# Optimization experiments

Hardware: AMD Instinct MI355X
Metric: run time of the kernel (lower is better)

## Reference

```python
import jax, jax.numpy as jnp
import numpy as np

IOU_THRESHOLD = 0.5


def setup_inputs() -> dict:
    key = jax.random.key(0)
    k1, k2, k3 = jax.random.split(key, 3)
    B, N = 4, 8192
    # valid boxes: top-left in [0,200), width/height in [1,51)
    xy = jax.random.uniform(k1, (B, N, 2), dtype=jnp.float32) * 200.0
    wh = jax.random.uniform(k2, (B, N, 2), dtype=jnp.float32) * 50.0 + 1.0
    boxes = jnp.concatenate([xy, xy + wh], axis=-1)  # [B,N,4] (x1,y1,x2,y2)
    scores = jax.random.uniform(k3, (B, N), dtype=jnp.float32)
    return {"boxes": boxes, "scores": scores}


def _soft_nms_single(boxes, scores):
    # boxes: [N,4], scores: [N]
    x1, y1, x2, y2 = boxes[:, 0], boxes[:, 1], boxes[:, 2], boxes[:, 3]
    inter_w = jnp.maximum(0.0, jnp.minimum(x2[:, None], x2[None, :]) - jnp.maximum(x1[:, None], x1[None, :]))
    inter_h = jnp.maximum(0.0, jnp.minimum(y2[:, None], y2[None, :]) - jnp.maximum(y1[:, None], y1[None, :]))
    inter = inter_w * inter_h  # [N,N]
    area = (x2 - x1) * (y2 - y1)  # [N]
    union = area[:, None] + area[None, :] - inter
    iou = inter / union  # [N,N]
    weight = jnp.exp(-iou / IOU_THRESHOLD)  # [N,N]
    adjusted = weight @ scores  # [N] : adjusted_scores[i] = sum_j w[i,j]*s[j]
    w = jax.nn.softmax(adjusted, axis=0)  # [N]
    return w @ boxes  # [4]


def reference(boxes, scores):
    return jax.vmap(_soft_nms_single)(boxes, scores)  # [B,4]
```

## Files before the change

kernel.cpp:

```cpp
#include <hip/hip_runtime.h>
#include <hip/hip_bf16.h>

#define BATCH   4
#define NBOX    8192
#define BLOCK   256
#define TSZ     256
#define NT      (NBOX / TSZ)
#define NPAIRS  (NT * (NT + 1) / 2)
#define NBINS   2048
#define SUBS    8
#define SUBSZ   (NBOX / SUBS)
#define STH     512

__device__ __forceinline__ float bf2f(unsigned short u) {
    union { unsigned int i; float f; } c;
    c.i = ((unsigned int)u) << 16;
    return c.f;
}

__device__ __forceinline__ bool box_plausible(float x1, float y1, float x2, float y2) {
    bool ok = (x1 == x1) && (y1 == y1) && (x2 == x2) && (y2 == y2);
    ok = ok && fabsf(x1) < 1e4f && fabsf(y1) < 1e4f && fabsf(x2) < 1e4f && fabsf(y2) < 1e4f;
    ok = ok && x1 >= -1.0f && x1 <= 300.0f && y1 >= -1.0f && y1 <= 300.0f;
    const float w = x2 - x1, h = y2 - y1;
    ok = ok && w >= -0.1f && w <= 80.0f && h >= -0.1f && h <= 80.0f;
    return ok;
}

__device__ __forceinline__ bool wave_probe_is_f32(const void* boxes_raw) {
    const int lane = threadIdx.x & 63;
    const float* bf = (const float*)boxes_raw;
    const bool okf = box_plausible(bf[lane * 4 + 0], bf[lane * 4 + 1],
                                   bf[lane * 4 + 2], bf[lane * 4 + 3]);
    const unsigned short* bh = (const unsigned short*)boxes_raw;
    const bool okh = box_plausible(bf2f(bh[lane * 4 + 0]), bf2f(bh[lane * 4 + 1]),
                                   bf2f(bh[lane * 4 + 2]), bf2f(bh[lane * 4 + 3]));
    const unsigned long long mf = __ballot(okf);
    const unsigned long long mh = __ballot(okh);
    return __popcll(mf) >= __popcll(mh);
}

__device__ __forceinline__ float4 load_box(const void* boxes_raw, size_t idx, bool isf32) {
    if (isf32) {
        return reinterpret_cast<const float4*>(boxes_raw)[idx];
    } else {
        const ushort4 u = reinterpret_cast<const ushort4*>(boxes_raw)[idx];
        return make_float4(bf2f(u.x), bf2f(u.y), bf2f(u.z), bf2f(u.w));
    }
}

__device__ __forceinline__ float load_score(const void* scores_raw, size_t idx, bool isf32) {
    return isf32 ? ((const float*)scores_raw)[idx]
                 : bf2f(((const unsigned short*)scores_raw)[idx]);
}

__device__ __forceinline__ int x1_bin(float x1) {
    const int bb = (int)(x1 * 8.0f);
    return min(NBINS - 1, max(0, bb));
}

#define CEXP (-2.8853900817779268f)

__device__ __forceinline__ float pair_weight(
    float ix1, float iy1, float ix2, float iy2, float iarea,
    const float4& bj, float jarea)
{
    float w = fminf(ix2, bj.z) - fmaxf(ix1, bj.x);
    float h = fminf(iy2, bj.w) - fmaxf(iy1, bj.y);
    w = fmaxf(w, 0.0f);
    h = fmaxf(h, 0.0f);
    const float inter = w * h;
    const float uni   = iarea + jarea - inter;
    const float arg   = (CEXP * inter) * __builtin_amdgcn_rcpf(uni);
    return __builtin_amdgcn_exp2f(arg);
}

__global__ __launch_bounds__(STH) void sort_kernel(
    const void* __restrict__ boxes_raw, const void* __restrict__ scores_raw,
    float4* __restrict__ sboxes, float* __restrict__ sscores,
    float* __restrict__ adj,
    float* __restrict__ minx1c, float* __restrict__ maxx2c,
    int* __restrict__ pairlist, int* __restrict__ count)
{
    __shared__ int hist[NBINS];
    __shared__ int bmax[NBINS];
    __shared__ int hist2[NBINS];
    __shared__ int wsum[STH / 64];
    __shared__ float sminT[NT], smaxT[NT];
    __shared__ int scnt;

    const int b    = blockIdx.x / SUBS;
    const int sub  = blockIdx.x % SUBS;
    const int tid  = threadIdx.x;
    const int lane = tid & 63;
    const int wv   = tid >> 6;
    const bool isf32 = wave_probe_is_f32(boxes_raw);
    const size_t base = (size_t)b * NBOX;

#pragma unroll
    for (int i = 0; i < NBINS / STH; i++) {
        hist[i * STH + tid]  = 0;
        bmax[i * STH + tid]  = 0;
        hist2[i * STH + tid] = 0;
    }
    if (tid == 0) scnt = 0;
    {
        const size_t z = (size_t)blockIdx.x * 1024;
        adj[z + tid] = 0.0f;
        adj[z + STH + tid] = 0.0f;
    }
    __syncthreads();

#pragma unroll
    for (int k = 0; k < NBOX / STH; k++) {
        const float4 bx = load_box(boxes_raw, base + k * STH + tid, isf32);
        const int bin = x1_bin(bx.x);
        atomicAdd(&hist[bin], 1);
        atomicMax(&bmax[bin], __float_as_int(bx.z));
    }
    for (int i = tid; i < sub * SUBSZ; i += STH) {
        const float4 bx = load_box(boxes_raw, base + i, isf32);
        atomicAdd(&hist2[x1_bin(bx.x)], 1);
    }
    __syncthreads();

    {
        int tot[4], cum[4];
        int run = 0;
#pragma unroll
        for (int i = 0; i < 4; i++) {
            tot[i] = hist[tid * 4 + i];
            run += tot[i]; cum[i] = run;
        }
        int v = run;
#pragma unroll
        for (int d = 1; d < 64; d <<= 1) {
            const int u = __shfl_up(v, d);
            if (lane >= d) v += u;
        }
        if (lane == 63) wsum[wv] = v;
        __syncthreads();
        int wb = 0;
        for (int w = 0; w < wv; w++) wb += wsum[w];
        const int tb = wb + v - run;
#pragma unroll
        for (int i = 0; i < 4; i++) {
            const int bin = tid * 4 + i;
            const int e = tb + cum[i] - tot[i];
            const int m = hist2[bin];
            hist[bin]  = e;
            hist2[bin] = e + m;
        }
    }
    __syncthreads();

    if (tid < NT) {
        int p = tid * TSZ;
        int lo = 0, hi = NBINS - 1;
        while (lo < hi) { const int mid = (lo + hi + 1) >> 1;
                          if (hist[mid] <= p) lo = mid; else hi = mid - 1; }
        const int Bf = lo;
        p = tid * TSZ + TSZ - 1;
        lo = 0; hi = NBINS - 1;
        while (lo < hi) { const int mid = (lo + hi + 1) >> 1;
                          if (hist[mid] <= p) lo = mid; else hi = mid - 1; }
        const int Bl = lo;
        int mb = 0;
        for (int q = Bf; q <= Bl; q++) mb = max(mb, bmax[q]);
        const float mn = (float)Bf * 0.125f;
        const float mx = __int_as_float(mb);
        sminT[tid] = mn; smaxT[tid] = mx;
        if (sub == 0) {
            minx1c[b * NT + tid] = mn;
            maxx2c[b * NT + tid] = mx;
        }
    }
    __syncthreads();

    if (sub == 0) {
        for (int q = tid; q < NPAIRS; q += STH) {
            int p = q, it = 0;
            while (p >= NT - it) { p -= NT - it; it++; }
            const int jt = it + p;
            const bool live = !((smaxT[it] < sminT[jt]) || (smaxT[jt] < sminT[it]));
            if (live) {
                const int idx = atomicAdd(&scnt, 1);
                pairlist[b * NPAIRS + idx] = (it << 8) | jt;
            }
        }
    }

#pragma unroll
    for (int k = 0; k < SUBSZ / STH; k++) {
        const int i = sub * SUBSZ + k * STH + tid;
        const float4 bx = load_box(boxes_raw, base + i, isf32);
        const float  sc = load_score(scores_raw, base + i, isf32);
        const int pos = atomicAdd(&hist2[x1_bin(bx.x)], 1);
        sboxes[base + pos]  = bx;
        sscores[base + pos] = sc;
    }

    __syncthreads();
    if (sub == 0 && tid == 0) count[b] = scnt;
}

__global__ __launch_bounds__(BLOCK, 4) void soft_nms_adj_kernel(
    const float4* __restrict__ sboxes,
    const float* __restrict__ sscores,
    const int* __restrict__ pairlist,
    const int* __restrict__ count,
    float* __restrict__ adj)
{
    __shared__ float4 sbox[TSZ];
    __shared__ float2 sas[TSZ];
    __shared__ float  srow[4][TSZ];

    const int bid = blockIdx.x;
    const int b   = bid / NPAIRS;
    const int p   = bid % NPAIRS;
    if (p >= count[b]) return;
    const int pr = pairlist[b * NPAIRS + p];
    const int it = pr >> 8, jt = pr & 255;

    const int tid  = threadIdx.x;
    const int lane = tid & 63;
    const int wv   = tid >> 6;
    const size_t base = (size_t)b * NBOX;

    {
        const int jg = jt * TSZ + tid;
        const float4 uj = sboxes[base + jg];
        sbox[tid] = uj;
        sas[tid]  = make_float2((uj.z - uj.x) * (uj.w - uj.y), sscores[base + jg]);
    }

    float rx1[4], ry1[4], rx2[4], ry2[4], rar[4], rsc[4], accr[4];
#pragma unroll
    for (int k = 0; k < 4; k++) {
        const int ig = it * TSZ + k * 64 + lane;
        const float4 ui = sboxes[base + ig];
        rx1[k] = ui.x; ry1[k] = ui.y; rx2[k] = ui.z; ry2[k] = ui.w;
        rar[k] = (ui.z - ui.x) * (ui.w - ui.y);
        rsc[k] = sscores[base + ig];
        accr[k] = 0.0f;
    }

    __syncthreads();

    const int wvbase = wv * 64;

    if (it == jt) {
#pragma unroll 2
        for (int t = 0; t < 64; t++) {
            const int idx = wvbase + ((lane + t) & 63);
            const float4 bj = sbox[idx];
            const float2 as = sas[idx];
#pragma unroll
            for (int k = 0; k < 4; k++) {
                const float e = pair_weight(rx1[k], ry1[k], rx2[k], ry2[k], rar[k], bj, as.x);
                accr[k] = fmaf(e, as.y, accr[k]);
            }
        }
    } else {
        float accc = 0.0f;
#pragma unroll 2
        for (int t = 0; t < 64; t++) {
            const int idx = wvbase + ((lane + t) & 63);
            const float4 bj = sbox[idx];
            const float2 as = sas[idx];
            const float e0 = pair_weight(rx1[0], ry1[0], rx2[0], ry2[0], rar[0], bj, as.x);
            const float e1 = pair_weight(rx1[1], ry1[1], rx2[1], ry2[1], rar[1], bj, as.x);
            const float e2 = pair_weight(rx1[2], ry1[2], rx2[2], ry2[2], rar[2], bj, as.x);
            const float e3 = pair_weight(rx1[3], ry1[3], rx2[3], ry2[3], rar[3], bj, as.x);
            accr[0] = fmaf(e0, as.y, accr[0]);
            accr[1] = fmaf(e1, as.y, accr[1]);
            accr[2] = fmaf(e2, as.y, accr[2]);
            accr[3] = fmaf(e3, as.y, accr[3]);
            const float c = fmaf(e0, rsc[0], fmaf(e1, rsc[1], fmaf(e2, rsc[2], e3 * rsc[3])));
            accc += __shfl(c, (lane - t) & 63);
        }
        atomicAdd(&adj[base + jt * TSZ + wvbase + lane], accc);
    }

#pragma unroll
    for (int k = 0; k < 4; k++) srow[wv][k * 64 + lane] = accr[k];
    __syncthreads();
    {
        const float rs = srow[0][tid] + srow[1][tid] + srow[2][tid] + srow[3][tid];
        atomicAdd(&adj[base + it * TSZ + tid], rs);
    }
}

#define FBLK 1024
__global__ __launch_bounds__(FBLK) void soft_nms_finish_kernel(
    const float4* __restrict__ sboxes,
    const float* __restrict__ sscores,
    const float* __restrict__ adj,
    const float* __restrict__ minx1c, const float* __restrict__ maxx2c,
    const void* __restrict__ boxes_raw,
    void* __restrict__ out)
{
    constexpr int K  = NBOX / FBLK;
    constexpr int NW = FBLK / 64;
    __shared__ float sminx[NT], smaxx[NT], ssumT[NT], scorr[NT];
    __shared__ float smax_[NW];
    __shared__ float sred[NW][5];

    const int b    = blockIdx.x;
    const int tid  = threadIdx.x;
    const int lane = tid & 63;
    const int wv   = tid >> 6;
    const size_t base = (size_t)b * NBOX;

    const bool isf32 = wave_probe_is_f32(boxes_raw);

    if (tid < NT) {
        sminx[tid] = minx1c[b * NT + tid];
        smaxx[tid] = maxx2c[b * NT + tid];
    }
#pragma unroll
    for (int tt = 0; tt < 2; tt++) {
        const int T = wv * 2 + tt;
        float sm = 0.0f;
#pragma unroll
        for (int q = 0; q < 4; q++) sm += sscores[base + T * TSZ + q * 64 + lane];
#pragma unroll
        for (int off = 32; off > 0; off >>= 1) sm += __shfl_down(sm, off);
        if (lane == 0) ssumT[T] = sm;
    }
    __syncthreads();
    if (tid < NT) {
        float c = 0.0f;
        for (int T2 = 0; T2 < NT; T2++) {
            const bool skip = (smaxx[tid] < sminx[T2]) || (smaxx[T2] < sminx[tid]);
            if (skip) c += ssumT[T2];
        }
        scorr[tid] = c;
    }
    __syncthreads();

    float av[K];
    float m = -3.4e38f;
#pragma unroll
    for (int k = 0; k < K; k++) {
        const int r = k * FBLK + tid;
        av[k] = adj[base + r] + scorr[r >> 8];
        m = fmaxf(m, av[k]);
    }
#pragma unroll
    for (int off = 32; off > 0; off >>= 1)
        m = fmaxf(m, __shfl_down(m, off));
    if (lane == 0) smax_[wv] = m;
    __syncthreads();
    float M = smax_[0];
#pragma unroll
    for (int w = 1; w < NW; w++) M = fmaxf(M, smax_[w]);

    const float L2E = 1.4426950408889634f;
    float es = 0.0f, s0 = 0.0f, s1 = 0.0f, s2 = 0.0f, s3 = 0.0f;
#pragma unroll
    for (int k = 0; k < K; k++) {
        const float e = __builtin_amdgcn_exp2f((av[k] - M) * L2E);
        const float4 u = sboxes[base + k * FBLK + tid];
        es += e;
        s0 += e * u.x;
        s1 += e * u.y;
        s2 += e * u.z;
        s3 += e * u.w;
    }
#pragma unroll
    for (int off = 32; off > 0; off >>= 1) {
        es += __shfl_down(es, off);
        s0 += __shfl_down(s0, off);
        s1 += __shfl_down(s1, off);
        s2 += __shfl_down(s2, off);
        s3 += __shfl_down(s3, off);
    }
    if (lane == 0) {
        sred[wv][0] = es; sred[wv][1] = s0; sred[wv][2] = s1;
        sred[wv][3] = s2; sred[wv][4] = s3;
    }
    __syncthreads();
    if (tid == 0) {
        float ES = 0.0f, o[4] = {0.0f, 0.0f, 0.0f, 0.0f};
#pragma unroll
        for (int w = 0; w < NW; w++) {
            ES   += sred[w][0];
            o[0] += sred[w][1];
            o[1] += sred[w][2];
            o[2] += sred[w][3];
            o[3] += sred[w][4];
        }
        const float inv = 1.0f / ES;
        if (isf32) {
            float* of = (float*)out;
            for (int c = 0; c < 4; c++) of[b * 4 + c] = o[c] * inv;
        } else {
            __hip_bfloat16* oh = (__hip_bfloat16*)out;
            for (int c = 0; c < 4; c++) oh[b * 4 + c] = __float2bfloat16(o[c] * inv);
        }
    }
}

extern "C" void kernel_launch(void* const* d_in, const int* in_sizes, int n_in,
                              void* d_out, int out_size, void* d_ws, size_t ws_size,
                              hipStream_t stream) {
    const void* boxes_raw  = d_in[0];
    const void* scores_raw = d_in[1];

    char* w = (char*)d_ws;
    float4* sboxes   = (float4*)w;                 w += (size_t)BATCH * NBOX * 16;
    float*  sscores  = (float*)w;                  w += (size_t)BATCH * NBOX * 4;
    float*  adj      = (float*)w;                  w += (size_t)BATCH * NBOX * 4;
    float*  minx1c   = (float*)w;                  w += (size_t)BATCH * NT * 4;
    float*  maxx2c   = (float*)w;                  w += (size_t)BATCH * NT * 4;
    int*    pairlist = (int*)w;                    w += (size_t)BATCH * NPAIRS * 4;
    int*    count    = (int*)w;

    sort_kernel<<<dim3(BATCH * SUBS), dim3(STH), 0, stream>>>(
        boxes_raw, scores_raw, sboxes, sscores, adj, minx1c, maxx2c, pairlist, count);
    soft_nms_adj_kernel<<<dim3(BATCH * NPAIRS), dim3(BLOCK), 0, stream>>>(
        sboxes, sscores, pairlist, count, adj);
    soft_nms_finish_kernel<<<dim3(BATCH), dim3(FBLK), 0, stream>>>(
        sboxes, sscores, adj, minx1c, maxx2c, boxes_raw, d_out);
}
```

Measured before the change: 121.9 us.

## Sort boxes by x2 and skip non-overlapping row groups in off-diagonal tiles

Switches the bucket sort key from x1 to x2, so tile bounds become a min-x1 per tile and a bin-derived max-x2. In off-diagonal tiles the kernel finds leading 64-row groups whose max x2 lies below the column tile's min x1. Those pairs have zero IoU and weight 1, so their contribution is added in closed form as score sums instead of evaluated pairwise. A templated loop then runs only over the remaining row groups, cutting exp and divide work at the cost of extra shuffles and code variants.

```diff
diff --git a/kernel.cpp b/kernel.cpp
--- a/kernel.cpp
+++ b/kernel.cpp
@@ -1,5 +1,6 @@
 #include <hip/hip_runtime.h>
 #include <hip/hip_bf16.h>
+#include <type_traits>
 
 #define BATCH   4
 #define NBOX    8192
@@ -54,8 +55,8 @@
                  : bf2f(((const unsigned short*)scores_raw)[idx]);
 }
 
-__device__ __forceinline__ int x1_bin(float x1) {
-    const int bb = (int)(x1 * 8.0f);
+__device__ __forceinline__ int key_bin(float v) {
+    const int bb = (int)(v * 8.0f);
     return min(NBINS - 1, max(0, bb));
 }
 
@@ -83,7 +84,7 @@
     int* __restrict__ pairlist, int* __restrict__ count)
 {
     __shared__ int hist[NBINS];
-    __shared__ int bmax[NBINS];
+    __shared__ int bmin[NBINS];
     __shared__ int hist2[NBINS];
     __shared__ int wsum[STH / 64];
     __shared__ float sminT[NT], smaxT[NT];
@@ -100,7 +101,7 @@
 #pragma unroll
     for (int i = 0; i < NBINS / STH; i++) {
         hist[i * STH + tid]  = 0;
-        bmax[i * STH + tid]  = 0;
+        bmin[i * STH + tid]  = 0x7f800000;
         hist2[i * STH + tid] = 0;
     }
     if (tid == 0) scnt = 0;
@@ -111,16 +112,15 @@
     }
     __syncthreads();
 
+    const int sublim = sub * SUBSZ;
 #pragma unroll
     for (int k = 0; k < NBOX / STH; k++) {
-        const float4 bx = load_box(boxes_raw, base + k * STH + tid, isf32);
-        const int bin = x1_bin(bx.x);
+        const int i = k * STH + tid;
+        const float4 bx = load_box(boxes_raw, base + i, isf32);
+        const int bin = key_bin(bx.z);
         atomicAdd(&hist[bin], 1);
-        atomicMax(&bmax[bin], __float_as_int(bx.z));
-    }
-    for (int i = tid; i < sub * SUBSZ; i += STH) {
-        const float4 bx = load_box(boxes_raw, base + i, isf32);
-        atomicAdd(&hist2[x1_bin(bx.x)], 1);
+        atomicMin(&bmin[bin], __float_as_int(bx.x));
+        if (i < sublim) atomicAdd(&hist2[bin], 1);
     }
     __syncthreads();
 
@@ -165,10 +165,9 @@
         while (lo < hi) { const int mid = (lo + hi + 1) >> 1;
                           if (hist[mid] <= p) lo = mid; else hi = mid - 1; }
         const int Bl = lo;
-        int mb = 0;
-        for (int q = Bf; q <= Bl; q++) mb = max(mb, bmax[q]);
-        const float mn = (float)Bf * 0.125f;
-        const float mx = __int_as_float(mb);
+        float mn = 3.4e38f;
+        for (int q = Bf; q <= Bl; q++) mn = fminf(mn, __int_as_float(bmin[q]));
+        const float mx = (float)(Bl + 1) * 0.125f;
         sminT[tid] = mn; smaxT[tid] = mx;
         if (sub == 0) {
             minx1c[b * NT + tid] = mn;
@@ -195,7 +194,7 @@
         const int i = sub * SUBSZ + k * STH + tid;
         const float4 bx = load_box(boxes_raw, base + i, isf32);
         const float  sc = load_score(scores_raw, base + i, isf32);
-        const int pos = atomicAdd(&hist2[x1_bin(bx.x)], 1);
+        const int pos = atomicAdd(&hist2[key_bin(bx.z)], 1);
         sboxes[base + pos]  = bx;
         sscores[base + pos] = sc;
     }
@@ -209,11 +208,13 @@
     const float* __restrict__ sscores,
     const int* __restrict__ pairlist,
     const int* __restrict__ count,
+    const float* __restrict__ minx1c,
     float* __restrict__ adj)
 {
     __shared__ float4 sbox[TSZ];
     __shared__ float2 sas[TSZ];
     __shared__ float  srow[4][TSZ];
+    __shared__ float  swsum[4];
 
     const int bid = blockIdx.x;
     const int b   = bid / NPAIRS;
@@ -231,10 +232,15 @@
         const int jg = jt * TSZ + tid;
         const float4 uj = sboxes[base + jg];
         sbox[tid] = uj;
-        sas[tid]  = make_float2((uj.z - uj.x) * (uj.w - uj.y), sscores[base + jg]);
-    }
-
-    float rx1[4], ry1[4], rx2[4], ry2[4], rar[4], rsc[4], accr[4];
+        const float jsc = sscores[base + jg];
+        sas[tid]  = make_float2((uj.z - uj.x) * (uj.w - uj.y), jsc);
+        float ws = jsc;
+#pragma unroll
+        for (int off = 32; off > 0; off >>= 1) ws += __shfl_xor(ws, off);
+        if (lane == 0) swsum[wv] = ws;
+    }
+
+    float rx1[4], ry1[4], rx2[4], ry2[4], rar[4], rsc[4];
 #pragma unroll
     for (int k = 0; k < 4; k++) {
         const int ig = it * TSZ + k * 64 + lane;
@@ -242,10 +248,36 @@
         rx1[k] = ui.x; ry1[k] = ui.y; rx2[k] = ui.z; ry2[k] = ui.w;
         rar[k] = (ui.z - ui.x) * (ui.w - ui.y);
         rsc[k] = sscores[base + ig];
-        accr[k] = 0.0f;
-    }
-
-    __syncthreads();
+    }
+
+    int kstart = 0;
+    if (it != jt) {
+        const float sminJ = minx1c[b * NT + jt];
+#pragma unroll
+        for (int k = 0; k < 4; k++) {
+            const float gmax = __shfl(rx2[k], 63) + 0.125f;
+            if (kstart == k && gmax < sminJ) kstart = k + 1;
+        }
+    }
+    float ccorr = 0.0f;
+    if (kstart > 0) {
+#pragma unroll
+        for (int k = 0; k < 4; k++) {
+            if (k < kstart) {
+                float gs = rsc[k];
+#pragma unroll
+                for (int off = 32; off > 0; off >>= 1) gs += __shfl_xor(gs, off);
+                ccorr += gs;
+            }
+        }
+    }
+
+    __syncthreads();
+
+    const float tilejsum = swsum[0] + swsum[1] + swsum[2] + swsum[3];
+    float accr[4];
+#pragma unroll
+    for (int k = 0; k < 4; k++) accr[k] = (k < kstart && wv == 0) ? tilejsum : 0.0f;
 
     const int wvbase = wv * 64;
 
@@ -262,24 +294,31 @@
             }
         }
     } else {
-        float accc = 0.0f;
+        auto offd = [&](auto KSC) {
+            constexpr int KS = decltype(KSC)::value;
+            float accc = ccorr;
 #pragma unroll 2
-        for (int t = 0; t < 64; t++) {
-            const int idx = wvbase + ((lane + t) & 63);
-            const float4 bj = sbox[idx];
-            const float2 as = sas[idx];
-            const float e0 = pair_weight(rx1[0], ry1[0], rx2[0], ry2[0], rar[0], bj, as.x);
-            const float e1 = pair_weight(rx1[1], ry1[1], rx2[1], ry2[1], rar[1], bj, as.x);
-            const float e2 = pair_weight(rx1[2], ry1[2], rx2[2], ry2[2], rar[2], bj, as.x);
-            const float e3 = pair_weight(rx1[3], ry1[3], rx2[3], ry2[3], rar[3], bj, as.x);
-            accr[0] = fmaf(e0, as.y, accr[0]);
-            accr[1] = fmaf(e1, as.y, accr[1]);
-            accr[2] = fmaf(e2, as.y, accr[2]);
-            accr[3] = fmaf(e3, as.y, accr[3]);
-            const float c = fmaf(e0, rsc[0], fmaf(e1, rsc[1], fmaf(e2, rsc[2], e3 * rsc[3])));
-            accc += __shfl(c, (lane - t) & 63);
-        }
-        atomicAdd(&adj[base + jt * TSZ + wvbase + lane], accc);
+            for (int t = 0; t < 64; t++) {
+                const int idx = wvbase + ((lane + t) & 63);
+                const float4 bj = sbox[idx];
+                const float2 as = sas[idx];
+                float c = 0.0f;
+#pragma unroll
+                for (int k = KS; k < 4; ++k) {
+                    const float e = pair_weight(rx1[k], ry1[k], rx2[k], ry2[k], rar[k], bj, as.x);
+                    accr[k] = fmaf(e, as.y, accr[k]);
+                    c = fmaf(e, rsc[k], c);
+                }
+                accc += __shfl(c, (lane - t) & 63);
+            }
+            atomicAdd(&adj[base + jt * TSZ + wvbase + lane], accc);
+        };
+        switch (kstart) {
+            case 0:  offd(std::integral_constant<int, 0>{}); break;
+            case 1:  offd(std::integral_constant<int, 1>{}); break;
+            case 2:  offd(std::integral_constant<int, 2>{}); break;
+            default: offd(std::integral_constant<int, 3>{}); break;
+        }
     }
 
 #pragma unroll
@@ -420,7 +459,7 @@
     sort_kernel<<<dim3(BATCH * SUBS), dim3(STH), 0, stream>>>(
         boxes_raw, scores_raw, sboxes, sscores, adj, minx1c, maxx2c, pairlist, count);
     soft_nms_adj_kernel<<<dim3(BATCH * NPAIRS), dim3(BLOCK), 0, stream>>>(
-        sboxes, sscores, pairlist, count, adj);
+        sboxes, sscores, pairlist, count, minx1c, adj);
     soft_nms_finish_kernel<<<dim3(BATCH), dim3(FBLK), 0, stream>>>(
         sboxes, sscores, adj, minx1c, maxx2c, boxes_raw, d_out);
 }
```

Result: slower. 135.5 us (+11.1%).

## Sort boxes by x2 key and split adjacency tiles into single-wave blocks

Applied to the files above, without the earlier changes.

The sort now bins boxes by x2 instead of x1, and tile bounds come from per-bin minimum x1 and the bin's upper x2 edge. The second-prefix histogram pass is folded into the main load loop. The adjacency kernel launches one 64-thread wave per quarter of a tile pair instead of a 256-thread block. This removes __syncthreads and the shared-memory row reduction, and aims for better load balance and occupancy. The cost is four times as many blocks, each reloading the row boxes, plus 4x more atomicAdds on the row accumulators.

```diff
diff --git a/kernel.cpp b/kernel.cpp
--- a/kernel.cpp
+++ b/kernel.cpp
@@ -3,10 +3,10 @@
 
 #define BATCH   4
 #define NBOX    8192
-#define BLOCK   256
 #define TSZ     256
 #define NT      (NBOX / TSZ)
 #define NPAIRS  (NT * (NT + 1) / 2)
+#define QSPLIT  4
 #define NBINS   2048
 #define SUBS    8
 #define SUBSZ   (NBOX / SUBS)
@@ -54,8 +54,8 @@
                  : bf2f(((const unsigned short*)scores_raw)[idx]);
 }
 
-__device__ __forceinline__ int x1_bin(float x1) {
-    const int bb = (int)(x1 * 8.0f);
+__device__ __forceinline__ int key_bin(float v) {
+    const int bb = (int)(v * 8.0f);
     return min(NBINS - 1, max(0, bb));
 }
 
@@ -83,7 +83,7 @@
     int* __restrict__ pairlist, int* __restrict__ count)
 {
     __shared__ int hist[NBINS];
-    __shared__ int bmax[NBINS];
+    __shared__ int bmin[NBINS];
     __shared__ int hist2[NBINS];
     __shared__ int wsum[STH / 64];
     __shared__ float sminT[NT], smaxT[NT];
@@ -100,7 +100,7 @@
 #pragma unroll
     for (int i = 0; i < NBINS / STH; i++) {
         hist[i * STH + tid]  = 0;
-        bmax[i * STH + tid]  = 0;
+        bmin[i * STH + tid]  = 0x7f800000;
         hist2[i * STH + tid] = 0;
     }
     if (tid == 0) scnt = 0;
@@ -111,16 +111,15 @@
     }
     __syncthreads();
 
+    const int sublim = sub * SUBSZ;
 #pragma unroll
     for (int k = 0; k < NBOX / STH; k++) {
-        const float4 bx = load_box(boxes_raw, base + k * STH + tid, isf32);
-        const int bin = x1_bin(bx.x);
+        const int i = k * STH + tid;
+        const float4 bx = load_box(boxes_raw, base + i, isf32);
+        const int bin = key_bin(bx.z);
         atomicAdd(&hist[bin], 1);
-        atomicMax(&bmax[bin], __float_as_int(bx.z));
-    }
-    for (int i = tid; i < sub * SUBSZ; i += STH) {
-        const float4 bx = load_box(boxes_raw, base + i, isf32);
-        atomicAdd(&hist2[x1_bin(bx.x)], 1);
+        atomicMin(&bmin[bin], __float_as_int(bx.x));
+        if (i < sublim) atomicAdd(&hist2[bin], 1);
     }
     __syncthreads();
 
@@ -165,10 +164,9 @@
         while (lo < hi) { const int mid = (lo + hi + 1) >> 1;
                           if (hist[mid] <= p) lo = mid; else hi = mid - 1; }
         const int Bl = lo;
-        int mb = 0;
-        for (int q = Bf; q <= Bl; q++) mb = max(mb, bmax[q]);
-        const float mn = (float)Bf * 0.125f;
-        const float mx = __int_as_float(mb);
+        float mn = 3.4e38f;
+        for (int q = Bf; q <= Bl; q++) mn = fminf(mn, __int_as_float(bmin[q]));
+        const float mx = (float)(Bl + 1) * 0.125f;
         sminT[tid] = mn; smaxT[tid] = mx;
         if (sub == 0) {
             minx1c[b * NT + tid] = mn;
@@ -195,7 +193,7 @@
         const int i = sub * SUBSZ + k * STH + tid;
         const float4 bx = load_box(boxes_raw, base + i, isf32);
         const float  sc = load_score(scores_raw, base + i, isf32);
-        const int pos = atomicAdd(&hist2[x1_bin(bx.x)], 1);
+        const int pos = atomicAdd(&hist2[key_bin(bx.z)], 1);
         sboxes[base + pos]  = bx;
         sscores[base + pos] = sc;
     }
@@ -204,34 +202,34 @@
     if (sub == 0 && tid == 0) count[b] = scnt;
 }
 
-__global__ __launch_bounds__(BLOCK, 4) void soft_nms_adj_kernel(
+__global__ __launch_bounds__(64, 8) void soft_nms_adj_kernel(
     const float4* __restrict__ sboxes,
     const float* __restrict__ sscores,
     const int* __restrict__ pairlist,
     const int* __restrict__ count,
     float* __restrict__ adj)
 {
-    __shared__ float4 sbox[TSZ];
-    __shared__ float2 sas[TSZ];
-    __shared__ float  srow[4][TSZ];
+    __shared__ float4 sbox[64];
+    __shared__ float2 sas[64];
 
     const int bid = blockIdx.x;
-    const int b   = bid / NPAIRS;
-    const int p   = bid % NPAIRS;
+    const int b   = bid / (NPAIRS * QSPLIT);
+    const int r   = bid % (NPAIRS * QSPLIT);
+    const int p   = r >> 2;
+    const int q   = r & 3;
     if (p >= count[b]) return;
     const int pr = pairlist[b * NPAIRS + p];
     const int it = pr >> 8, jt = pr & 255;
 
-    const int tid  = threadIdx.x;
-    const int lane = tid & 63;
-    const int wv   = tid >> 6;
+    const int lane = threadIdx.x;
     const size_t base = (size_t)b * NBOX;
+    const int colg = jt * TSZ + q * 64;
 
     {
-        const int jg = jt * TSZ + tid;
-        const float4 uj = sboxes[base + jg];
-        sbox[tid] = uj;
-        sas[tid]  = make_float2((uj.z - uj.x) * (uj.w - uj.y), sscores[base + jg]);
+        const float4 uj = sboxes[base + colg + lane];
+        sbox[lane] = uj;
+        sas[lane]  = make_float2((uj.z - uj.x) * (uj.w - uj.y),
+                                 sscores[base + colg + lane]);
     }
 
     float rx1[4], ry1[4], rx2[4], ry2[4], rar[4], rsc[4], accr[4];
@@ -245,14 +243,10 @@
         accr[k] = 0.0f;
     }
 
-    __syncthreads();
-
-    const int wvbase = wv * 64;
-
     if (it == jt) {
 #pragma unroll 2
         for (int t = 0; t < 64; t++) {
-            const int idx = wvbase + ((lane + t) & 63);
+            const int idx = (lane + t) & 63;
             const float4 bj = sbox[idx];
             const float2 as = sas[idx];
 #pragma unroll
@@ -265,7 +259,7 @@
         float accc = 0.0f;
 #pragma unroll 2
         for (int t = 0; t < 64; t++) {
-            const int idx = wvbase + ((lane + t) & 63);
+            const int idx = (lane + t) & 63;
             const float4 bj = sbox[idx];
             const float2 as = sas[idx];
             const float e0 = pair_weight(rx1[0], ry1[0], rx2[0], ry2[0], rar[0], bj, as.x);
@@ -279,16 +273,12 @@
             const float c = fmaf(e0, rsc[0], fmaf(e1, rsc[1], fmaf(e2, rsc[2], e3 * rsc[3])));
             accc += __shfl(c, (lane - t) & 63);
         }
-        atomicAdd(&adj[base + jt * TSZ + wvbase + lane], accc);
-    }
-
-#pragma unroll
-    for (int k = 0; k < 4; k++) srow[wv][k * 64 + lane] = accr[k];
-    __syncthreads();
-    {
-        const float rs = srow[0][tid] + srow[1][tid] + srow[2][tid] + srow[3][tid];
-        atomicAdd(&adj[base + it * TSZ + tid], rs);
-    }
+        atomicAdd(&adj[base + colg + lane], accc);
+    }
+
+#pragma unroll
+    for (int k = 0; k < 4; k++)
+        atomicAdd(&adj[base + it * TSZ + k * 64 + lane], accr[k]);
 }
 
 #define FBLK 1024
@@ -419,7 +409,7 @@
 
     sort_kernel<<<dim3(BATCH * SUBS), dim3(STH), 0, stream>>>(
         boxes_raw, scores_raw, sboxes, sscores, adj, minx1c, maxx2c, pairlist, count);
-    soft_nms_adj_kernel<<<dim3(BATCH * NPAIRS), dim3(BLOCK), 0, stream>>>(
+    soft_nms_adj_kernel<<<dim3(BATCH * NPAIRS * QSPLIT), dim3(64), 0, stream>>>(
         sboxes, sscores, pairlist, count, adj);
     soft_nms_finish_kernel<<<dim3(BATCH), dim3(FBLK), 0, stream>>>(
         sboxes, sscores, adj, minx1c, maxx2c, boxes_raw, d_out);
```

After: 130.3 us. 6.9% more time.

## Fuse softmax finish into adj kernel via last-block-done counter; merge histogram passes

Applied to the files above, without the earlier changes.

The separate finish kernel is removed. Each adj block now increments a per-batch done counter after a threadfence, and the last block to finish computes the tile correction, softmax and weighted box sum. This saves one kernel launch and its gap, but the final reduction now runs on a 256-thread block instead of 1024 threads. The sort kernel also builds its prefix histogram inside the main pass instead of re-reading boxes in a second loop.

```diff
diff --git a/kernel.cpp b/kernel.cpp
--- a/kernel.cpp
+++ b/kernel.cpp
@@ -80,7 +80,8 @@
     float4* __restrict__ sboxes, float* __restrict__ sscores,
     float* __restrict__ adj,
     float* __restrict__ minx1c, float* __restrict__ maxx2c,
-    int* __restrict__ pairlist, int* __restrict__ count)
+    int* __restrict__ pairlist, int* __restrict__ count,
+    int* __restrict__ done)
 {
     __shared__ int hist[NBINS];
     __shared__ int bmax[NBINS];
@@ -104,6 +105,7 @@
         hist2[i * STH + tid] = 0;
     }
     if (tid == 0) scnt = 0;
+    if (sub == 0 && tid == 0) done[b] = 0;
     {
         const size_t z = (size_t)blockIdx.x * 1024;
         adj[z + tid] = 0.0f;
@@ -111,16 +113,15 @@
     }
     __syncthreads();
 
+    const int sublim = sub * SUBSZ;
 #pragma unroll
     for (int k = 0; k < NBOX / STH; k++) {
-        const float4 bx = load_box(boxes_raw, base + k * STH + tid, isf32);
+        const int i = k * STH + tid;
+        const float4 bx = load_box(boxes_raw, base + i, isf32);
         const int bin = x1_bin(bx.x);
         atomicAdd(&hist[bin], 1);
         atomicMax(&bmax[bin], __float_as_int(bx.z));
-    }
-    for (int i = tid; i < sub * SUBSZ; i += STH) {
-        const float4 bx = load_box(boxes_raw, base + i, isf32);
-        atomicAdd(&hist2[x1_bin(bx.x)], 1);
+        if (i < sublim) atomicAdd(&hist2[bin], 1);
     }
     __syncthreads();
 
@@ -209,159 +210,147 @@
     const float* __restrict__ sscores,
     const int* __restrict__ pairlist,
     const int* __restrict__ count,
-    float* __restrict__ adj)
+    const float* __restrict__ minx1c, const float* __restrict__ maxx2c,
+    const void* __restrict__ boxes_raw,
+    float* __restrict__ adj,
+    int* __restrict__ done,
+    void* __restrict__ out)
 {
     __shared__ float4 sbox[TSZ];
     __shared__ float2 sas[TSZ];
     __shared__ float  srow[4][TSZ];
+    __shared__ int    sord;
+    __shared__ float fsminx[NT], fsmaxx[NT], fssum[NT], fscorr[NT];
+    __shared__ float fsmax[4];
+    __shared__ float fred[4][5];
 
     const int bid = blockIdx.x;
     const int b   = bid / NPAIRS;
     const int p   = bid % NPAIRS;
-    if (p >= count[b]) return;
-    const int pr = pairlist[b * NPAIRS + p];
-    const int it = pr >> 8, jt = pr & 255;
-
     const int tid  = threadIdx.x;
     const int lane = tid & 63;
     const int wv   = tid >> 6;
     const size_t base = (size_t)b * NBOX;
 
-    {
-        const int jg = jt * TSZ + tid;
-        const float4 uj = sboxes[base + jg];
-        sbox[tid] = uj;
-        sas[tid]  = make_float2((uj.z - uj.x) * (uj.w - uj.y), sscores[base + jg]);
-    }
-
-    float rx1[4], ry1[4], rx2[4], ry2[4], rar[4], rsc[4], accr[4];
-#pragma unroll
-    for (int k = 0; k < 4; k++) {
-        const int ig = it * TSZ + k * 64 + lane;
-        const float4 ui = sboxes[base + ig];
-        rx1[k] = ui.x; ry1[k] = ui.y; rx2[k] = ui.z; ry2[k] = ui.w;
-        rar[k] = (ui.z - ui.x) * (ui.w - ui.y);
-        rsc[k] = sscores[base + ig];
-        accr[k] = 0.0f;
-    }
-
-    __syncthreads();
-
-    const int wvbase = wv * 64;
-
-    if (it == jt) {
+    if (p < count[b]) {
+        const int pr = pairlist[b * NPAIRS + p];
+        const int it = pr >> 8, jt = pr & 255;
+
+        {
+            const int jg = jt * TSZ + tid;
+            const float4 uj = sboxes[base + jg];
+            sbox[tid] = uj;
+            sas[tid]  = make_float2((uj.z - uj.x) * (uj.w - uj.y), sscores[base + jg]);
+        }
+
+        float rx1[4], ry1[4], rx2[4], ry2[4], rar[4], rsc[4], accr[4];
+#pragma unroll
+        for (int k = 0; k < 4; k++) {
+            const int ig = it * TSZ + k * 64 + lane;
+            const float4 ui = sboxes[base + ig];
+            rx1[k] = ui.x; ry1[k] = ui.y; rx2[k] = ui.z; ry2[k] = ui.w;
+            rar[k] = (ui.z - ui.x) * (ui.w - ui.y);
+            rsc[k] = sscores[base + ig];
+            accr[k] = 0.0f;
+        }
+
+        __syncthreads();
+
+        const int wvbase = wv * 64;
+
+        if (it == jt) {
 #pragma unroll 2
-        for (int t = 0; t < 64; t++) {
-            const int idx = wvbase + ((lane + t) & 63);
-            const float4 bj = sbox[idx];
-            const float2 as = sas[idx];
-#pragma unroll
-            for (int k = 0; k < 4; k++) {
-                const float e = pair_weight(rx1[k], ry1[k], rx2[k], ry2[k], rar[k], bj, as.x);
-                accr[k] = fmaf(e, as.y, accr[k]);
+            for (int t = 0; t < 64; t++) {
+                const int idx = wvbase + ((lane + t) & 63);
+                const float4 bj = sbox[idx];
+                const float2 as = sas[idx];
+#pragma unroll
+                for (int k = 0; k < 4; k++) {
+                    const float e = pair_weight(rx1[k], ry1[k], rx2[k], ry2[k], rar[k], bj, as.x);
+                    accr[k] = fmaf(e, as.y, accr[k]);
+                }
             }
-        }
-    } else {
-        float accc = 0.0f;
+        } else {
+            float accc = 0.0f;
 #pragma unroll 2
-        for (int t = 0; t < 64; t++) {
-            const int idx = wvbase + ((lane + t) & 63);
-            const float4 bj = sbox[idx];
-            const float2 as = sas[idx];
-            const float e0 = pair_weight(rx1[0], ry1[0], rx2[0], ry2[0], rar[0], bj, as.x);
-            const float e1 = pair_weight(rx1[1], ry1[1], rx2[1], ry2[1], rar[1], bj, as.x);
-            const float e2 = pair_weight(rx1[2], ry1[2], rx2[2], ry2[2], rar[2], bj, as.x);
-            const float e3 = pair_weight(rx1[3], ry1[3], rx2[3], ry2[3], rar[3], bj, as.x);
-            accr[0] = fmaf(e0, as.y, accr[0]);
-            accr[1] = fmaf(e1, as.y, accr[1]);
-            accr[2] = fmaf(e2, as.y, accr[2]);
-            accr[3] = fmaf(e3, as.y, accr[3]);
-            const float c = fmaf(e0, rsc[0], fmaf(e1, rsc[1], fmaf(e2, rsc[2], e3 * rsc[3])));
-            accc += __shfl(c, (lane - t) & 63);
-        }
-        atomicAdd(&adj[base + jt * TSZ + wvbase + lane], accc);
-    }
-
-#pragma unroll
-    for (int k = 0; k < 4; k++) srow[wv][k * 64 + lane] = accr[k];
-    __syncthreads();
-    {
-        const float rs = srow[0][tid] + srow[1][tid] + srow[2][tid] + srow[3][tid];
-        atomicAdd(&adj[base + it * TSZ + tid], rs);
-    }
-}
-
-#define FBLK 1024
-__global__ __launch_bounds__(FBLK) void soft_nms_finish_kernel(
-    const float4* __restrict__ sboxes,
-    const float* __restrict__ sscores,
-    const float* __restrict__ adj,
-    const float* __restrict__ minx1c, const float* __restrict__ maxx2c,
-    const void* __restrict__ boxes_raw,
-    void* __restrict__ out)
-{
-    constexpr int K  = NBOX / FBLK;
-    constexpr int NW = FBLK / 64;
-    __shared__ float sminx[NT], smaxx[NT], ssumT[NT], scorr[NT];
-    __shared__ float smax_[NW];
-    __shared__ float sred[NW][5];
-
-    const int b    = blockIdx.x;
-    const int tid  = threadIdx.x;
-    const int lane = tid & 63;
-    const int wv   = tid >> 6;
-    const size_t base = (size_t)b * NBOX;
+            for (int t = 0; t < 64; t++) {
+                const int idx = wvbase + ((lane + t) & 63);
+                const float4 bj = sbox[idx];
+                const float2 as = sas[idx];
+                const float e0 = pair_weight(rx1[0], ry1[0], rx2[0], ry2[0], rar[0], bj, as.x);
+                const float e1 = pair_weight(rx1[1], ry1[1], rx2[1], ry2[1], rar[1], bj, as.x);
+                const float e2 = pair_weight(rx1[2], ry1[2], rx2[2], ry2[2], rar[2], bj, as.x);
+                const float e3 = pair_weight(rx1[3], ry1[3], rx2[3], ry2[3], rar[3], bj, as.x);
+                accr[0] = fmaf(e0, as.y, accr[0]);
+                accr[1] = fmaf(e1, as.y, accr[1]);
+                accr[2] = fmaf(e2, as.y, accr[2]);
+                accr[3] = fmaf(e3, as.y, accr[3]);
+                const float c = fmaf(e0, rsc[0], fmaf(e1, rsc[1], fmaf(e2, rsc[2], e3 * rsc[3])));
+                accc += __shfl(c, (lane - t) & 63);
+            }
+            atomicAdd(&adj[base + jt * TSZ + wvbase + lane], accc);
+        }
+
+#pragma unroll
+        for (int k = 0; k < 4; k++) srow[wv][k * 64 + lane] = accr[k];
+        __syncthreads();
+        {
+            const float rs = srow[0][tid] + srow[1][tid] + srow[2][tid] + srow[3][tid];
+            atomicAdd(&adj[base + it * TSZ + tid], rs);
+        }
+    }
+
+    __threadfence();
+    if (tid == 0) sord = atomicAdd(&done[b], 1);
+    __syncthreads();
+    if (sord != NPAIRS - 1) return;
+    __threadfence();
 
     const bool isf32 = wave_probe_is_f32(boxes_raw);
 
     if (tid < NT) {
-        sminx[tid] = minx1c[b * NT + tid];
-        smaxx[tid] = maxx2c[b * NT + tid];
-    }
-#pragma unroll
-    for (int tt = 0; tt < 2; tt++) {
-        const int T = wv * 2 + tt;
+        fsminx[tid] = minx1c[b * NT + tid];
+        fsmaxx[tid] = maxx2c[b * NT + tid];
+    }
+#pragma unroll
+    for (int tt = 0; tt < NT / 4; tt++) {
+        const int T = wv * (NT / 4) + tt;
         float sm = 0.0f;
 #pragma unroll
         for (int q = 0; q < 4; q++) sm += sscores[base + T * TSZ + q * 64 + lane];
 #pragma unroll
         for (int off = 32; off > 0; off >>= 1) sm += __shfl_down(sm, off);
-        if (lane == 0) ssumT[T] = sm;
+        if (lane == 0) fssum[T] = sm;
     }
     __syncthreads();
     if (tid < NT) {
         float c = 0.0f;
         for (int T2 = 0; T2 < NT; T2++) {
-            const bool skip = (smaxx[tid] < sminx[T2]) || (smaxx[T2] < sminx[tid]);
-            if (skip) c += ssumT[T2];
-        }
-        scorr[tid] = c;
-    }
-    __syncthreads();
-
-    float av[K];
+            const bool skip = (fsmaxx[tid] < fsminx[T2]) || (fsmaxx[T2] < fsminx[tid]);
+            if (skip) c += fssum[T2];
+        }
+        fscorr[tid] = c;
+    }
+    __syncthreads();
+
     float m = -3.4e38f;
-#pragma unroll
-    for (int k = 0; k < K; k++) {
-        const int r = k * FBLK + tid;
-        av[k] = adj[base + r] + scorr[r >> 8];
-        m = fmaxf(m, av[k]);
-    }
+#pragma unroll 4
+    for (int k = 0; k < NBOX / BLOCK; k++)
+        m = fmaxf(m, adj[base + k * BLOCK + tid] + fscorr[k]);
 #pragma unroll
     for (int off = 32; off > 0; off >>= 1)
         m = fmaxf(m, __shfl_down(m, off));
-    if (lane == 0) smax_[wv] = m;
-    __syncthreads();
-    float M = smax_[0];
-#pragma unroll
-    for (int w = 1; w < NW; w++) M = fmaxf(M, smax_[w]);
+    if (lane == 0) fsmax[wv] = m;
+    __syncthreads();
+    const float M = fmaxf(fmaxf(fsmax[0], fsmax[1]), fmaxf(fsmax[2], fsmax[3]));
 
     const float L2E = 1.4426950408889634f;
     float es = 0.0f, s0 = 0.0f, s1 = 0.0f, s2 = 0.0f, s3 = 0.0f;
-#pragma unroll
-    for (int k = 0; k < K; k++) {
-        const float e = __builtin_amdgcn_exp2f((av[k] - M) * L2E);
-        const float4 u = sboxes[base + k * FBLK + tid];
+#pragma unroll 4
+    for (int k = 0; k < NBOX / BLOCK; k++) {
+        const size_t r = base + k * BLOCK + tid;
+        const float e = __builtin_amdgcn_exp2f((adj[r] + fscorr[k] - M) * L2E);
+        const float4 u = sboxes[r];
         es += e;
         s0 += e * u.x;
         s1 += e * u.y;
@@ -377,19 +366,19 @@
         s3 += __shfl_down(s3, off);
     }
     if (lane == 0) {
-        sred[wv][0] = es; sred[wv][1] = s0; sred[wv][2] = s1;
-        sred[wv][3] = s2; sred[wv][4] = s3;
+        fred[wv][0] = es; fred[wv][1] = s0; fred[wv][2] = s1;
+        fred[wv][3] = s2; fred[wv][4] = s3;
     }
     __syncthreads();
     if (tid == 0) {
         float ES = 0.0f, o[4] = {0.0f, 0.0f, 0.0f, 0.0f};
 #pragma unroll
-        for (int w = 0; w < NW; w++) {
-            ES   += sred[w][0];
-            o[0] += sred[w][1];
-            o[1] += sred[w][2];
-            o[2] += sred[w][3];
-            o[3] += sred[w][4];
+        for (int w = 0; w < 4; w++) {
+            ES   += fred[w][0];
+            o[0] += fred[w][1];
+            o[1] += fred[w][2];
+            o[2] += fred[w][3];
+            o[3] += fred[w][4];
         }
         const float inv = 1.0f / ES;
         if (isf32) {
@@ -415,12 +404,13 @@
     float*  minx1c   = (float*)w;                  w += (size_t)BATCH * NT * 4;
     float*  maxx2c   = (float*)w;                  w += (size_t)BATCH * NT * 4;
     int*    pairlist = (int*)w;                    w += (size_t)BATCH * NPAIRS * 4;
-    int*    count    = (int*)w;
+    int*    count    = (int*)w;                    w += (size_t)BATCH * 4;
+    int*    done     = (int*)w;
 
     sort_kernel<<<dim3(BATCH * SUBS), dim3(STH), 0, stream>>>(
-        boxes_raw, scores_raw, sboxes, sscores, adj, minx1c, maxx2c, pairlist, count);
+        boxes_raw, scores_raw, sboxes, sscores, adj, minx1c, maxx2c,
+        pairlist, count, done);
     soft_nms_adj_kernel<<<dim3(BATCH * NPAIRS), dim3(BLOCK), 0, stream>>>(
-        sboxes, sscores, pairlist, count, adj);
-    soft_nms_finish_kernel<<<dim3(BATCH), dim3(FBLK), 0, stream>>>(
-        sboxes, sscores, adj, minx1c, maxx2c, boxes_raw, d_out);
-}
+        sboxes, sscores, pairlist, count, minx1c, maxx2c, boxes_raw,
+        adj, done, d_out);
+}
```

New measurement: 214.6 us. 76.0% more time.
